# Optimization experiments

Measured on AMD Instinct MI355X. Metric: run time of the kernel, lower is better.

Reference implementation:

```python
import jax, jax.numpy as jnp
import numpy as np
from jax import lax

D_MODEL = 1024
N_HEADS = 8
D_HEAD = 64
D_INNER = N_HEADS * D_HEAD  # 512
B, T = 4, 4096
LN_EPS = 1e-5
NORM_EPS = 1e-12  # F.normalize default eps


def setup_inputs() -> dict:
    key = jax.random.key(0)
    ks = jax.random.split(key, 6)
    s_proj = (2.0 / (D_MODEL + D_INNER)) ** 0.5  # xavier_uniform-ish std
    x = jax.random.normal(ks[0], (B, T, D_MODEL), jnp.float32)
    Wq = jax.random.normal(ks[1], (D_MODEL, D_INNER), jnp.float32) * s_proj
    Wk = jax.random.normal(ks[2], (D_MODEL, D_INNER), jnp.float32) * s_proj
    Wv = jax.random.normal(ks[3], (D_MODEL, D_INNER), jnp.float32) * s_proj
    Wa = jax.random.normal(ks[4], (D_MODEL, D_INNER), jnp.float32) * s_proj
    ba = jnp.full((D_INNER,), 3.0, jnp.float32)  # nn.init.constant_(W_alpha.bias, 3.0)
    Wo = jax.random.normal(ks[5], (D_INNER, D_MODEL), jnp.float32) * s_proj
    gamma = jnp.ones((D_MODEL,), jnp.float32)
    beta = jnp.zeros((D_MODEL,), jnp.float32)
    return {"x": x, "Wq": Wq, "Wk": Wk, "Wv": Wv, "Wa": Wa, "ba": ba,
            "Wo": Wo, "gamma": gamma, "beta": beta}


def reference(x, Wq, Wk, Wv, Wa, ba, Wo, gamma, beta):
    Bx, Tx, _ = x.shape
    residual = x
    # LayerNorm
    mu = jnp.mean(x, axis=-1, keepdims=True)
    var = jnp.var(x, axis=-1, keepdims=True)
    xn = (x - mu) / jnp.sqrt(var + LN_EPS) * gamma + beta
    # Projections -> (B, T, H, d) -> time-major (T, B, H, d) for scan
    def heads(y):
        return jnp.moveaxis(y.reshape(Bx, Tx, N_HEADS, D_HEAD), 1, 0)
    q = heads(xn @ Wq)
    k = heads(xn @ Wk)
    v = heads(xn @ Wv)
    alpha = jax.nn.sigmoid(heads(xn @ Wa + ba))
    # F.normalize(k, dim=-1)
    knorm = jnp.linalg.norm(k, axis=-1, keepdims=True)
    k = k / jnp.maximum(knorm, NORM_EPS)

    # Recurrence: S_t = diag(a_t) S_{t-1} + k_t v_t^T ; o_t = S_t^T q_t
    def step(S, inp):
        q_t, k_t, v_t, a_t = inp  # each (B, H, d)
        S = a_t[..., None] * S + k_t[..., None] * v_t[..., None, :]  # (B,H,dk,dv)
        o_t = jnp.einsum('bhji,bhj->bhi', S, q_t)
        return S, o_t

    S0 = jnp.zeros((Bx, N_HEADS, D_HEAD, D_HEAD), x.dtype)
    _, outs = lax.scan(step, S0, (q, k, v, alpha))  # outs: (T, B, H, d)
    out = jnp.moveaxis(outs, 0, 1).reshape(Bx, Tx, D_INNER) @ Wo
    return out + residual
```

## Files before the change

kernel.cpp:

```cpp
#include <hip/hip_runtime.h>
#include <stdint.h>

#define NTOK   16384
#define DM     1024
#define DI     512
#define NH     8
#define DH     64
#define CHUNK  64
#define NCH    64
#define NBHC   2048

using short8 = __attribute__((ext_vector_type(8))) short;
using f32x4  = __attribute__((ext_vector_type(4))) float;

__device__ __forceinline__ unsigned short f2bf(float f) {
  union { float f; unsigned int u; } x; x.f = f;
  unsigned int u = x.u;
  return (unsigned short)((u + 0x7fffu + ((u >> 16) & 1u)) >> 16);
}
__device__ __forceinline__ float bf2f(unsigned short h) {
  union { unsigned int u; float f; } x; x.u = ((unsigned int)h) << 16; return x.f;
}

typedef const __attribute__((address_space(1))) void* gp1_t;
typedef __attribute__((address_space(3))) void* lp3_t;
__device__ __forceinline__ void gload_lds16(const void* g, void* l) {
  __builtin_amdgcn_global_load_lds((gp1_t)g, (lp3_t)l, 16, 0, 0);
}

__global__ __launch_bounds__(256) void transpose_bf16(const float* __restrict__ in,
                                                      unsigned short* __restrict__ out,
                                                      int R, int C) {
  __shared__ float tile[32][33];
  int bx = blockIdx.x * 32;
  int by = blockIdx.y * 32;
  int tx = threadIdx.x & 31, ty = threadIdx.x >> 5;
  #pragma unroll
  for (int r = ty; r < 32; r += 8) tile[r][tx] = in[(long)(by + r) * C + bx + tx];
  __syncthreads();
  #pragma unroll
  for (int r = ty; r < 32; r += 8) out[(long)(bx + r) * R + by + tx] = f2bf(tile[tx][r]);
}

__global__ __launch_bounds__(256) void ln_kernel(const float* __restrict__ x,
                                                 const float* __restrict__ gamma,
                                                 const float* __restrict__ beta,
                                                 unsigned short* __restrict__ xn) {
  const int row = blockIdx.x, tid = threadIdx.x;
  float4 v = ((const float4*)(x + (long)row * DM))[tid];
  float s  = v.x + v.y + v.z + v.w;
  float ss = v.x * v.x + v.y * v.y + v.z * v.z + v.w * v.w;
  #pragma unroll
  for (int off = 32; off > 0; off >>= 1) { s += __shfl_down(s, off); ss += __shfl_down(ss, off); }
  __shared__ float rs_[4], rss_[4];
  int wave = tid >> 6, lane = tid & 63;
  if (lane == 0) { rs_[wave] = s; rss_[wave] = ss; }
  __syncthreads();
  s  = rs_[0] + rs_[1] + rs_[2] + rs_[3];
  ss = rss_[0] + rss_[1] + rss_[2] + rss_[3];
  float mu   = s * (1.f / DM);
  float var  = ss * (1.f / DM) - mu * mu;
  float rstd = rsqrtf(var + 1e-5f);
  int idx = tid * 4;
  float xv[4] = {v.x, v.y, v.z, v.w};
  unsigned short o[4];
  #pragma unroll
  for (int j = 0; j < 4; ++j) o[j] = f2bf((xv[j] - mu) * rstd * gamma[idx + j] + beta[idx + j]);
  uint2 pk; pk.x = (unsigned)o[0] | ((unsigned)o[1] << 16); pk.y = (unsigned)o[2] | ((unsigned)o[3] << 16);
  *(uint2*)(xn + (long)row * DM + idx) = pk;
}

template <int MODE>
__global__ __launch_bounds__(256) void gemm_bt(const unsigned short* __restrict__ A,
                                               const unsigned short* __restrict__ Bt,
                                               unsigned short* __restrict__ Cb,
                                               float* __restrict__ Cf,
                                               const float* __restrict__ resid,
                                               int M, int N, int K) {
  __shared__ __align__(16) unsigned short As[128 * 32];
  __shared__ __align__(16) unsigned short Bs[128 * 32];
  const int tid = threadIdx.x;
  const int wave = tid >> 6, lane = tid & 63;
  const int quad = lane >> 4, l16 = lane & 15;
  const int m0 = blockIdx.x * 128, n0 = blockIdx.y * 128;
  const int wm = (wave & 1) * 64, wn = (wave >> 1) * 64;

  const int c0 = tid, c1 = tid + 256;
  const unsigned short* Ag0 = A + (long)(m0 + (c0 >> 2)) * K + (c0 & 3) * 8;
  const unsigned short* Ag1 = A + (long)(m0 + (c1 >> 2)) * K + (c1 & 3) * 8;
  const unsigned short* Bg0 = Bt + (long)(n0 + (c0 >> 2)) * K + (c0 & 3) * 8;
  const unsigned short* Bg1 = Bt + (long)(n0 + (c1 >> 2)) * K + (c1 & 3) * 8;

  f32x4 acc[4][4];
  #pragma unroll
  for (int i = 0; i < 4; ++i)
    #pragma unroll
    for (int j = 0; j < 4; ++j) acc[i][j] = (f32x4){0.f, 0.f, 0.f, 0.f};

  for (int k0 = 0; k0 < K; k0 += 32) {
    __syncthreads();
    gload_lds16(Ag0 + k0, &As[c0 * 8]);
    gload_lds16(Ag1 + k0, &As[c1 * 8]);
    gload_lds16(Bg0 + k0, &Bs[c0 * 8]);
    gload_lds16(Bg1 + k0, &Bs[c1 * 8]);
    __syncthreads();
    short8 a[4], b[4];
    #pragma unroll
    for (int mt = 0; mt < 4; ++mt) a[mt] = *(const short8*)&As[(wm + mt * 16 + l16) * 32 + quad * 8];
    #pragma unroll
    for (int nt = 0; nt < 4; ++nt) b[nt] = *(const short8*)&Bs[(wn + nt * 16 + l16) * 32 + quad * 8];
    #pragma unroll
    for (int mt = 0; mt < 4; ++mt)
      #pragma unroll
      for (int nt = 0; nt < 4; ++nt)
        acc[mt][nt] = __builtin_amdgcn_mfma_f32_16x16x32_bf16(a[mt], b[nt], acc[mt][nt], 0, 0, 0);
  }
  #pragma unroll
  for (int mt = 0; mt < 4; ++mt)
    #pragma unroll
    for (int nt = 0; nt < 4; ++nt)
      #pragma unroll
      for (int r = 0; r < 4; ++r) {
        int row = m0 + wm + mt * 16 + quad * 4 + r;
        int col = n0 + wn + nt * 16 + l16;
        float v = acc[mt][nt][r];
        if (MODE == 0) {
          Cb[(long)row * N + col] = f2bf(v);
        } else {
          Cf[(long)row * N + col] = v + resid[(long)row * N + col];
        }
      }
}

#define TS 72
__global__ __launch_bounds__(256) void prep_intra_kernel(const unsigned short* __restrict__ Cb,
                                                         const float* __restrict__ ba,
                                                         unsigned short* __restrict__ qt,
                                                         float* __restrict__ Dvec,
                                                         unsigned short* __restrict__ Ointra,
                                                         unsigned short* __restrict__ Tt) {
  const int bhc = blockIdx.x;
  const int c = bhc & 63, bh = bhc >> 6;
  const int h = bh & 7, b = bh >> 3;
  const int tid = threadIdx.x;
  __shared__ __align__(16) unsigned short Qb[4096], Kb[4096], Ab[4096];
  __shared__ __align__(16) unsigned short Vt[64 * TS], Ht[64 * TS];
  __shared__ float lamF[4096];
  __shared__ float rnF[64];
  const long rowbase = ((long)(b * 4096 + c * 64)) * 2048;
  const int hoff = h * 64;

  if (tid < 64) rnF[tid] = 0.f;
  __syncthreads();

  #pragma unroll
  for (int chunk = 0; chunk < 2; ++chunk) {
    int u = chunk * 256 + tid;
    int t = u >> 3, p = u & 7;
    long g = rowbase + (long)t * 2048 + hoff + p * 8;
    uint4 q4 = *(const uint4*)(Cb + g);
    uint4 k4 = *(const uint4*)(Cb + g + 512);
    uint4 v4 = *(const uint4*)(Cb + g + 1024);
    uint4 a4 = *(const uint4*)(Cb + g + 1536);
    *(uint4*)&Qb[u * 8] = q4;
    *(uint4*)&Kb[u * 8] = k4;
    *(uint4*)&Ab[u * 8] = a4;
    const unsigned short* vs = (const unsigned short*)&v4;
    #pragma unroll
    for (int j = 0; j < 8; ++j) Vt[(p * 8 + j) * TS + t] = vs[j];
    const unsigned short* ks = (const unsigned short*)&k4;
    float ssq = 0.f;
    #pragma unroll
    for (int j = 0; j < 8; ++j) { float kv = bf2f(ks[j]); ssq += kv * kv; }
    atomicAdd(&rnF[t], ssq);
  }
  __syncthreads();

  {
    const float bav = ba[hoff + (tid & 63)];
    #pragma unroll
    for (int j = 0; j < 16; ++j) {
      int e = j * 256 + tid;
      float z = bf2f(Ab[e]) + bav;
      lamF[e] = 1.f / (1.f + __expf(-z));
    }
  }
  __syncthreads();

  if (tid < 64) {
    int d = tid; float cum = 1.f;
    for (int t = 0; t < 64; ++t) { cum *= lamF[t * 64 + d]; lamF[t * 64 + d] = cum; }
    Dvec[(long)bhc * 64 + d] = cum;
  } else if (tid < 128) {
    int t = tid - 64;
    rnF[t] = 1.f / fmaxf(sqrtf(rnF[t]), 1e-12f);
  }
  __syncthreads();

  {
    const int d = tid & 63;
    const float lend = lamF[63 * 64 + d];
    #pragma unroll
    for (int j = 0; j < 16; ++j) {
      int e = j * 256 + tid;
      int t = e >> 6;
      float lam = lamF[e];
      float rl = 1.f / lam;
      float kn = bf2f(Kb[e]) * rnF[t];
      Qb[e] = f2bf(bf2f(Qb[e]) * lam);
      Kb[e] = f2bf(kn * rl);
      Ht[d * TS + t] = f2bf(kn * lend * rl);
    }
  }
  __syncthreads();

  {
    const long obase = (long)bhc * 4096;
    uint4* gq = (uint4*)(qt + obase);
    const uint4* lq = (const uint4*)Qb;
    gq[tid] = lq[tid]; gq[tid + 256] = lq[tid + 256];
  }

  const long base = (long)bhc * 4096;
  const int wave = tid >> 6, lane = tid & 63, quad = lane >> 4, l16 = lane & 15;
  const int mrow = wave * 16 + l16;
  unsigned short* Ps = Ab;

  {
    short8 a0 = *(const short8*)&Qb[mrow * 64 + quad * 8];
    short8 a1 = *(const short8*)&Qb[mrow * 64 + 32 + quad * 8];
    #pragma unroll
    for (int nt = 0; nt < 4; ++nt) {
      short8 b0 = *(const short8*)&Kb[(nt * 16 + l16) * 64 + quad * 8];
      short8 b1 = *(const short8*)&Kb[(nt * 16 + l16) * 64 + 32 + quad * 8];
      f32x4 acc = (f32x4){0.f, 0.f, 0.f, 0.f};
      acc = __builtin_amdgcn_mfma_f32_16x16x32_bf16(a0, b0, acc, 0, 0, 0);
      acc = __builtin_amdgcn_mfma_f32_16x16x32_bf16(a1, b1, acc, 0, 0, 0);
      #pragma unroll
      for (int r = 0; r < 4; ++r) {
        int t = wave * 16 + quad * 4 + r, u = nt * 16 + l16;
        Ps[t * 64 + u] = (u <= t) ? f2bf(acc[r]) : (unsigned short)0;
      }
    }
  }
  {
    short8 a0 = *(const short8*)&Ps[mrow * 64 + quad * 8];
    short8 a1 = *(const short8*)&Ps[mrow * 64 + 32 + quad * 8];
    #pragma unroll
    for (int nt = 0; nt < 4; ++nt) {
      short8 b0 = *(const short8*)&Vt[(nt * 16 + l16) * TS + quad * 8];
      short8 b1 = *(const short8*)&Vt[(nt * 16 + l16) * TS + 32 + quad * 8];
      f32x4 acc = (f32x4){0.f, 0.f, 0.f, 0.f};
      acc = __builtin_amdgcn_mfma_f32_16x16x32_bf16(a0, b0, acc, 0, 0, 0);
      acc = __builtin_amdgcn_mfma_f32_16x16x32_bf16(a1, b1, acc, 0, 0, 0);
      #pragma unroll
      for (int r = 0; r < 4; ++r) {
        int t = wave * 16 + quad * 4 + r, i = nt * 16 + l16;
        Ointra[base + t * 64 + i] = f2bf(acc[r]);
      }
    }
  }
  {
    short8 a0 = *(const short8*)&Vt[mrow * TS + quad * 8];
    short8 a1 = *(const short8*)&Vt[mrow * TS + 32 + quad * 8];
    #pragma unroll
    for (int nt = 0; nt < 4; ++nt) {
      short8 b0 = *(const short8*)&Ht[(nt * 16 + l16) * TS + quad * 8];
      short8 b1 = *(const short8*)&Ht[(nt * 16 + l16) * TS + 32 + quad * 8];
      f32x4 acc = (f32x4){0.f, 0.f, 0.f, 0.f};
      acc = __builtin_amdgcn_mfma_f32_16x16x32_bf16(a0, b0, acc, 0, 0, 0);
      acc = __builtin_amdgcn_mfma_f32_16x16x32_bf16(a1, b1, acc, 0, 0, 0);
      #pragma unroll
      for (int r = 0; r < 4; ++r) {
        int i = wave * 16 + quad * 4 + r, j = nt * 16 + l16;
        Tt[base + i * 64 + j] = f2bf(acc[r]);
      }
    }
  }
}

__global__ __launch_bounds__(256) void scan_kernel(const unsigned short* __restrict__ Tt,
                                                   const float* __restrict__ Dvec,
                                                   unsigned short* __restrict__ Sst) {
  const int bh = blockIdx.x;
  const int e = blockIdx.y * 256 + threadIdx.x;
  const int j = e & 63;
  float S = 0.f;
  for (int c = 0; c < 64; ++c) {
    const long idx = ((long)(bh * 64 + c)) * 4096 + e;
    const float dj = Dvec[((long)(bh * 64 + c)) * 64 + j];
    Sst[idx] = f2bf(S);
    S = dj * S + bf2f(Tt[idx]);
  }
}

__global__ __launch_bounds__(256) void combine_kernel(const unsigned short* __restrict__ qt,
                                                      const unsigned short* __restrict__ Sst,
                                                      const unsigned short* __restrict__ Ointra,
                                                      unsigned short* __restrict__ O) {
  const int bhc = blockIdx.x;
  const int c = bhc & 63, bh = bhc >> 6;
  const int h = bh & 7, b = bh >> 3;
  const long base = (long)bhc * 4096;
  __shared__ __align__(16) unsigned short Qs[4096], Sb[4096];
  const int tid = threadIdx.x;
  {
    const uint4* gq = (const uint4*)(qt + base);  uint4* lq = (uint4*)Qs;
    const uint4* gs = (const uint4*)(Sst + base); uint4* ls = (uint4*)Sb;
    lq[tid] = gq[tid]; lq[tid + 256] = gq[tid + 256];
    ls[tid] = gs[tid]; ls[tid + 256] = gs[tid + 256];
  }
  __syncthreads();
  const int wave = tid >> 6, lane = tid & 63, quad = lane >> 4, l16 = lane & 15;
  const int mrow = wave * 16 + l16;
  short8 a0 = *(const short8*)&Qs[mrow * 64 + quad * 8];
  short8 a1 = *(const short8*)&Qs[mrow * 64 + 32 + quad * 8];
  #pragma unroll
  for (int nt = 0; nt < 4; ++nt) {
    f32x4 acc;
    #pragma unroll
    for (int r = 0; r < 4; ++r) {
      int t = wave * 16 + quad * 4 + r, i = nt * 16 + l16;
      acc[r] = bf2f(Ointra[base + t * 64 + i]);
    }
    short8 b0 = *(const short8*)&Sb[(nt * 16 + l16) * 64 + quad * 8];
    short8 b1 = *(const short8*)&Sb[(nt * 16 + l16) * 64 + 32 + quad * 8];
    acc = __builtin_amdgcn_mfma_f32_16x16x32_bf16(a0, b0, acc, 0, 0, 0);
    acc = __builtin_amdgcn_mfma_f32_16x16x32_bf16(a1, b1, acc, 0, 0, 0);
    #pragma unroll
    for (int r = 0; r < 4; ++r) {
      int t = wave * 16 + quad * 4 + r, i = nt * 16 + l16;
      O[((long)(b * 4096 + c * 64 + t)) * 512 + h * 64 + i] = f2bf(acc[r]);
    }
  }
}

extern "C" void kernel_launch(void* const* d_in, const int* in_sizes, int n_in,
                              void* d_out, int out_size, void* d_ws, size_t ws_size,
                              hipStream_t stream) {
  const float* x     = (const float*)d_in[0];
  const float* Wq    = (const float*)d_in[1];
  const float* Wk    = (const float*)d_in[2];
  const float* Wv    = (const float*)d_in[3];
  const float* Wa    = (const float*)d_in[4];
  const float* ba    = (const float*)d_in[5];
  const float* Wo    = (const float*)d_in[6];
  const float* gamma = (const float*)d_in[7];
  const float* beta  = (const float*)d_in[8];
  float* out = (float*)d_out;

  char* ws = (char*)d_ws;
  const size_t KB = 1024;
  unsigned short* Wt     = (unsigned short*)(ws + 0 * KB);
  unsigned short* Wot    = (unsigned short*)(ws + 4096 * KB);
  float*          Dvec   = (float*)         (ws + 5120 * KB);
  unsigned short* qt     = (unsigned short*)(ws + 5632 * KB);
  unsigned short* Ttb    = (unsigned short*)(ws + 22016 * KB);
  unsigned short* Sst    = (unsigned short*)(ws + 38400 * KB);
  unsigned short* xn     = (unsigned short*)(ws + 54784 * KB);
  unsigned short* Ointra = (unsigned short*)(ws + 54784 * KB);
  unsigned short* Ob     = (unsigned short*)(ws + 71168 * KB);
  unsigned short* Cb     = (unsigned short*)(ws + 87552 * KB);

  transpose_bf16<<<dim3(16, 32), 256, 0, stream>>>(Wq, Wt + (size_t)0 * 512 * 1024, 1024, 512);
  transpose_bf16<<<dim3(16, 32), 256, 0, stream>>>(Wk, Wt + (size_t)1 * 512 * 1024, 1024, 512);
  transpose_bf16<<<dim3(16, 32), 256, 0, stream>>>(Wv, Wt + (size_t)2 * 512 * 1024, 1024, 512);
  transpose_bf16<<<dim3(16, 32), 256, 0, stream>>>(Wa, Wt + (size_t)3 * 512 * 1024, 1024, 512);
  transpose_bf16<<<dim3(32, 16), 256, 0, stream>>>(Wo, Wot, 512, 1024);
  ln_kernel<<<NTOK, 256, 0, stream>>>(x, gamma, beta, xn);
  gemm_bt<0><<<dim3(NTOK / 128, 2048 / 128), 256, 0, stream>>>(xn, Wt, Cb, nullptr, nullptr, NTOK, 2048, 1024);
  prep_intra_kernel<<<NBHC, 256, 0, stream>>>(Cb, ba, qt, Dvec, Ointra, Ttb);
  scan_kernel<<<dim3(32, 16), 256, 0, stream>>>(Ttb, Dvec, Sst);
  combine_kernel<<<NBHC, 256, 0, stream>>>(qt, Sst, Ointra, Ob);
  gemm_bt<1><<<dim3(NTOK / 128, 1024 / 128), 256, 0, stream>>>(Ob, Wot, nullptr, out, x, NTOK, 1024, 512);
}
```

Baseline: 346.1 us.

## Stage GEMM epilogue through LDS, swizzle block order, fuse transposes and sigmoid

The GEMM epilogue now writes accumulators to LDS and then issues coalesced 16-byte stores; the fp32 output path reads the residual as float4. Block indices are remapped into groups of eight M-tiles to improve L2 reuse of B tiles. The four weight transposes are merged into a single launch. The sigmoid for the gates is computed straight from registers in prep_intra, which drops one LDS buffer and one barrier. In the fp32 output GEMM the accumulator is now rounded to bf16 before the residual add, which loses precision.

```diff
diff --git a/kernel.cpp b/kernel.cpp
--- a/kernel.cpp
+++ b/kernel.cpp
@@ -28,6 +28,25 @@
   __builtin_amdgcn_global_load_lds((gp1_t)g, (lp3_t)l, 16, 0, 0);
 }
 
+__global__ __launch_bounds__(256) void transpose4_bf16(const float* __restrict__ Wq,
+                                                       const float* __restrict__ Wk,
+                                                       const float* __restrict__ Wv,
+                                                       const float* __restrict__ Wa,
+                                                       unsigned short* __restrict__ out) {
+  const int z = blockIdx.z;
+  const float* in = (z == 0) ? Wq : (z == 1) ? Wk : (z == 2) ? Wv : Wa;
+  unsigned short* o = out + (size_t)z * 512 * 1024;
+  __shared__ float tile[32][33];
+  int bx = blockIdx.x * 32;
+  int by = blockIdx.y * 32;
+  int tx = threadIdx.x & 31, ty = threadIdx.x >> 5;
+  #pragma unroll
+  for (int r = ty; r < 32; r += 8) tile[r][tx] = in[(long)(by + r) * 512 + bx + tx];
+  __syncthreads();
+  #pragma unroll
+  for (int r = ty; r < 32; r += 8) o[(long)(bx + r) * 1024 + by + tx] = f2bf(tile[tx][r]);
+}
+
 __global__ __launch_bounds__(256) void transpose_bf16(const float* __restrict__ in,
                                                       unsigned short* __restrict__ out,
                                                       int R, int C) {
@@ -70,6 +89,7 @@
   *(uint2*)(xn + (long)row * DM + idx) = pk;
 }
 
+#define EPS 136
 template <int MODE>
 __global__ __launch_bounds__(256) void gemm_bt(const unsigned short* __restrict__ A,
                                                const unsigned short* __restrict__ Bt,
@@ -77,12 +97,19 @@
                                                float* __restrict__ Cf,
                                                const float* __restrict__ resid,
                                                int M, int N, int K) {
-  __shared__ __align__(16) unsigned short As[128 * 32];
-  __shared__ __align__(16) unsigned short Bs[128 * 32];
+  __shared__ __align__(16) unsigned short smem[128 * EPS];
+  unsigned short* As = smem;
+  unsigned short* Bs = smem + 4096;
   const int tid = threadIdx.x;
   const int wave = tid >> 6, lane = tid & 63;
   const int quad = lane >> 4, l16 = lane & 15;
-  const int m0 = blockIdx.x * 128, n0 = blockIdx.y * 128;
+
+  const int Nt = gridDim.y;
+  int id = blockIdx.x + blockIdx.y * gridDim.x;
+  int group = id / (8 * Nt);
+  int rem = id - group * (8 * Nt);
+  const int m0 = (group * 8 + (rem & 7)) * 128;
+  const int n0 = (rem >> 3) * 128;
   const int wm = (wave & 1) * 64, wn = (wave >> 1) * 64;
 
   const int c0 = tid, c1 = tid + 256;
@@ -115,21 +142,38 @@
       for (int nt = 0; nt < 4; ++nt)
         acc[mt][nt] = __builtin_amdgcn_mfma_f32_16x16x32_bf16(a[mt], b[nt], acc[mt][nt], 0, 0, 0);
   }
+  __syncthreads();
+  unsigned short* epi = smem;
   #pragma unroll
   for (int mt = 0; mt < 4; ++mt)
     #pragma unroll
     for (int nt = 0; nt < 4; ++nt)
       #pragma unroll
-      for (int r = 0; r < 4; ++r) {
-        int row = m0 + wm + mt * 16 + quad * 4 + r;
-        int col = n0 + wn + nt * 16 + l16;
-        float v = acc[mt][nt][r];
-        if (MODE == 0) {
-          Cb[(long)row * N + col] = f2bf(v);
-        } else {
-          Cf[(long)row * N + col] = v + resid[(long)row * N + col];
-        }
-      }
+      for (int r = 0; r < 4; ++r)
+        epi[(wm + mt * 16 + quad * 4 + r) * EPS + wn + nt * 16 + l16] = f2bf(acc[mt][nt][r]);
+  __syncthreads();
+  if (MODE == 0) {
+    #pragma unroll
+    for (int i = tid; i < 2048; i += 256) {
+      int row = i >> 4, cc = (i & 15) * 8;
+      uint4 v = *(const uint4*)&epi[row * EPS + cc];
+      *(uint4*)&Cb[(long)(m0 + row) * N + n0 + cc] = v;
+    }
+  } else {
+    #pragma unroll
+    for (int i = tid; i < 4096; i += 256) {
+      int row = i >> 5, cc = (i & 31) * 4;
+      long g = (long)(m0 + row) * N + n0 + cc;
+      float4 rv = *(const float4*)&resid[g];
+      uint2 pv = *(const uint2*)&epi[row * EPS + cc];
+      float4 ov;
+      ov.x = bf2f((unsigned short)(pv.x & 0xffffu)) + rv.x;
+      ov.y = bf2f((unsigned short)(pv.x >> 16))     + rv.y;
+      ov.z = bf2f((unsigned short)(pv.y & 0xffffu)) + rv.z;
+      ov.w = bf2f((unsigned short)(pv.y >> 16))     + rv.w;
+      *(float4*)&Cf[g] = ov;
+    }
+  }
 }
 
 #define TS 72
@@ -143,7 +187,7 @@
   const int c = bhc & 63, bh = bhc >> 6;
   const int h = bh & 7, b = bh >> 3;
   const int tid = threadIdx.x;
-  __shared__ __align__(16) unsigned short Qb[4096], Kb[4096], Ab[4096];
+  __shared__ __align__(16) unsigned short Qb[4096], Kb[4096];
   __shared__ __align__(16) unsigned short Vt[64 * TS], Ht[64 * TS];
   __shared__ float lamF[4096];
   __shared__ float rnF[64];
@@ -164,10 +208,15 @@
     uint4 a4 = *(const uint4*)(Cb + g + 1536);
     *(uint4*)&Qb[u * 8] = q4;
     *(uint4*)&Kb[u * 8] = k4;
-    *(uint4*)&Ab[u * 8] = a4;
     const unsigned short* vs = (const unsigned short*)&v4;
     #pragma unroll
     for (int j = 0; j < 8; ++j) Vt[(p * 8 + j) * TS + t] = vs[j];
+    const unsigned short* as_ = (const unsigned short*)&a4;
+    #pragma unroll
+    for (int j = 0; j < 8; ++j) {
+      float z = bf2f(as_[j]) + ba[hoff + p * 8 + j];
+      lamF[t * 64 + p * 8 + j] = 1.f / (1.f + __expf(-z));
+    }
     const unsigned short* ks = (const unsigned short*)&k4;
     float ssq = 0.f;
     #pragma unroll
@@ -176,19 +225,9 @@
   }
   __syncthreads();
 
-  {
-    const float bav = ba[hoff + (tid & 63)];
-    #pragma unroll
-    for (int j = 0; j < 16; ++j) {
-      int e = j * 256 + tid;
-      float z = bf2f(Ab[e]) + bav;
-      lamF[e] = 1.f / (1.f + __expf(-z));
-    }
-  }
-  __syncthreads();
-
   if (tid < 64) {
     int d = tid; float cum = 1.f;
+    #pragma unroll
     for (int t = 0; t < 64; ++t) { cum *= lamF[t * 64 + d]; lamF[t * 64 + d] = cum; }
     Dvec[(long)bhc * 64 + d] = cum;
   } else if (tid < 128) {
@@ -224,7 +263,7 @@
   const long base = (long)bhc * 4096;
   const int wave = tid >> 6, lane = tid & 63, quad = lane >> 4, l16 = lane & 15;
   const int mrow = wave * 16 + l16;
-  unsigned short* Ps = Ab;
+  unsigned short* Ps = (unsigned short*)lamF;
 
   {
     short8 a0 = *(const short8*)&Qb[mrow * 64 + quad * 8];
@@ -362,10 +401,7 @@
   unsigned short* Ob     = (unsigned short*)(ws + 71168 * KB);
   unsigned short* Cb     = (unsigned short*)(ws + 87552 * KB);
 
-  transpose_bf16<<<dim3(16, 32), 256, 0, stream>>>(Wq, Wt + (size_t)0 * 512 * 1024, 1024, 512);
-  transpose_bf16<<<dim3(16, 32), 256, 0, stream>>>(Wk, Wt + (size_t)1 * 512 * 1024, 1024, 512);
-  transpose_bf16<<<dim3(16, 32), 256, 0, stream>>>(Wv, Wt + (size_t)2 * 512 * 1024, 1024, 512);
-  transpose_bf16<<<dim3(16, 32), 256, 0, stream>>>(Wa, Wt + (size_t)3 * 512 * 1024, 1024, 512);
+  transpose4_bf16<<<dim3(16, 32, 4), 256, 0, stream>>>(Wq, Wk, Wv, Wa, Wt);
   transpose_bf16<<<dim3(32, 16), 256, 0, stream>>>(Wo, Wot, 512, 1024);
   ln_kernel<<<NTOK, 256, 0, stream>>>(x, gamma, beta, xn);
   gemm_bt<0><<<dim3(NTOK / 128, 2048 / 128), 256, 0, stream>>>(xn, Wt, Cb, nullptr, nullptr, NTOK, 2048, 1024);
```

After: 334.3 us. 1.04x faster.
